# Optimization experiments

Measured on AMD Instinct MI355X. Metric: run time of the kernel, lower is better.

The kernel has to match this reference:

```python
import jax, jax.numpy as jnp
import numpy as np

B, T, C = 4, 2048, 1024
NH = 16
HD = C // NH  # 64


def setup_inputs() -> dict:
    key = jax.random.key(0)
    k1, k2, k3, k4, k5 = jax.random.split(key, 5)
    s_in = 1.0 / np.sqrt(C)
    return {
        "x": jax.random.normal(k1, (B, T, C), dtype=jnp.float32),
        "attention_mask": jnp.ones((B, T), dtype=jnp.float32),
        "W_qkv": jax.random.normal(k2, (C, 3 * C), dtype=jnp.float32) * s_in,
        "b_qkv": jnp.zeros((3 * C,), dtype=jnp.float32),
        "W_out": jax.random.normal(k3, (C, C), dtype=jnp.float32) * s_in,
        "b_out": jnp.zeros((C,), dtype=jnp.float32),
    }


def reference(x, attention_mask, W_qkv, b_qkv, W_out, b_out):
    Bx, Tx, Cx = x.shape
    # QKV projection: (B,T,3C)
    qkv = x @ W_qkv + b_qkv
    Q, K, V = jnp.split(qkv, 3, axis=-1)
    # (B, NH, T, HD)
    Q = Q.reshape(Bx, Tx, NH, HD).transpose(0, 2, 1, 3)
    K = K.reshape(Bx, Tx, NH, HD).transpose(0, 2, 1, 3)
    V = V.reshape(Bx, Tx, NH, HD).transpose(0, 2, 1, 3)
    # scaled scores (B, NH, T, T)
    scores = jnp.einsum("bhqd,bhkd->bhqk", Q, K) * (1.0 / np.sqrt(HD))
    # causal mask: set strictly-upper triangle to -inf (mask-fill semantics)
    causal = jnp.tril(jnp.ones((Tx, Tx), dtype=bool))[None, None]
    scores = jnp.where(causal, scores, -jnp.inf)
    # additive padding mask
    pad = (1.0 - attention_mask)[:, None, None, :] * jnp.finfo(scores.dtype).min
    scores = scores + pad
    attn = jax.nn.softmax(scores, axis=-1)
    # weighted values -> (B, T, C)
    wv = jnp.einsum("bhqk,bhkd->bhqd", attn, V)
    wv = wv.transpose(0, 2, 1, 3).reshape(Bx, Tx, Cx)
    return wv @ W_out + b_out
```

## Files before the change

kernel.cpp:

```cpp
#include <hip/hip_runtime.h>
#include <math.h>

constexpr int BB = 4;
constexpr int TT = 2048;
constexpr int CC = 1024;
constexpr int NHH = 16;
constexpr int HDD = 64;
constexpr int C3 = 3 * CC;

typedef __bf16 bf16x8 __attribute__((ext_vector_type(8)));
typedef float  f32x4  __attribute__((ext_vector_type(4)));

__device__ __forceinline__ unsigned short f2bf(float x) {
    union { float f; unsigned u; } v; v.f = x;
    unsigned r = v.u + 0x7fffu + ((v.u >> 16) & 1u);
    return (unsigned short)(r >> 16);
}

#define AS1(p) ((const __attribute__((address_space(1))) void*)(p))
#define AS3(p) ((__attribute__((address_space(3))) void*)(p))

__global__ __launch_bounds__(256) void cast_bf16(
    const float* __restrict__ src, unsigned short* __restrict__ dst, int n4)
{
    int i = blockIdx.x * 256 + threadIdx.x;
    if (i < n4) {
        float4 v = ((const float4*)src)[i];
        ushort4 o;
        o.x = f2bf(v.x); o.y = f2bf(v.y); o.z = f2bf(v.z); o.w = f2bf(v.w);
        ((ushort4*)dst)[i] = o;
    }
}

__global__ __launch_bounds__(256) void transpose_cast(
    const float* __restrict__ src, unsigned short* __restrict__ dst,
    int R, int Cn)
{
    __shared__ float tile[64][65];
    const int r0 = blockIdx.y * 64, c0 = blockIdx.x * 64;
    const int t = threadIdx.x;
    const int lr = t >> 4, lc = (t & 15) * 4;
    #pragma unroll
    for (int s = 0; s < 4; ++s) {
        float4 v = *(const float4*)&src[(size_t)(r0 + lr + s * 16) * Cn + c0 + lc];
        tile[lr + s * 16][lc + 0] = v.x;
        tile[lr + s * 16][lc + 1] = v.y;
        tile[lr + s * 16][lc + 2] = v.z;
        tile[lr + s * 16][lc + 3] = v.w;
    }
    __syncthreads();
    const int oi = t >> 2, oc = (t & 3) * 16;
    unsigned short buf[16];
    #pragma unroll
    for (int u = 0; u < 16; ++u)
        buf[u] = f2bf(tile[oc + u][oi]);
    unsigned short* d = &dst[(size_t)(c0 + oi) * R + r0 + oc];
    *(uint4*)(d + 0) = *(uint4*)&buf[0];
    *(uint4*)(d + 8) = *(uint4*)&buf[8];
}

template<bool BF16OUT, bool VSPLIT>
__global__ __launch_bounds__(256) void gemm_bt_mfma(
    const unsigned short* __restrict__ A,
    const unsigned short* __restrict__ Bt,
    const float* __restrict__ bias,
    void* __restrict__ OutV,
    unsigned short* __restrict__ Vt_g,
    int M, int N, int K, int scale_n, float scale)
{
    __shared__ alignas(16) unsigned short As[128 * 32];
    __shared__ alignas(16) unsigned short Bs[128 * 32];

    const int tid  = threadIdx.x;
    const int w    = tid >> 6;
    const int lane = tid & 63;
    const int quad = lane >> 4;
    const int col  = lane & 15;
    const int m0 = blockIdx.y * 128, n0 = blockIdx.x * 128;
    const int wr = w >> 1, wc = w & 1;

    f32x4 acc[4][4];
    #pragma unroll
    for (int i = 0; i < 4; ++i)
        #pragma unroll
        for (int j = 0; j < 4; ++j)
            #pragma unroll
            for (int r = 0; r < 4; ++r)
                acc[i][j][r] = 0.0f;

    const int sr = tid >> 2;
    const int sc = (tid & 3) * 8;
    char* AsB = (char*)As;
    char* BsB = (char*)Bs;

    const unsigned short* Ag0 = A  + (size_t)(m0 + sr) * K + sc;
    const unsigned short* Ag1 = A  + (size_t)(m0 + 64 + sr) * K + sc;
    const unsigned short* Bg0 = Bt + (size_t)(n0 + sr) * K + sc;
    const unsigned short* Bg1 = Bt + (size_t)(n0 + 64 + sr) * K + sc;

    for (int k0 = 0; k0 < K; k0 += 32) {
        if (k0) __syncthreads();
        __builtin_amdgcn_global_load_lds(AS1(Ag0 + k0), AS3(AsB + w * 1024),        16, 0, 0);
        __builtin_amdgcn_global_load_lds(AS1(Ag1 + k0), AS3(AsB + 4096 + w * 1024), 16, 0, 0);
        __builtin_amdgcn_global_load_lds(AS1(Bg0 + k0), AS3(BsB + w * 1024),        16, 0, 0);
        __builtin_amdgcn_global_load_lds(AS1(Bg1 + k0), AS3(BsB + 4096 + w * 1024), 16, 0, 0);
        __syncthreads();

        bf16x8 af[4], bf[4];
        #pragma unroll
        for (int i = 0; i < 4; ++i) {
            af[i] = *(const bf16x8*)&As[(wr * 64 + i * 16 + col) * 32 + quad * 8];
            bf[i] = *(const bf16x8*)&Bs[(wc * 64 + i * 16 + col) * 32 + quad * 8];
        }
        #pragma unroll
        for (int i = 0; i < 4; ++i)
            #pragma unroll
            for (int j = 0; j < 4; ++j)
                acc[i][j] = __builtin_amdgcn_mfma_f32_16x16x32_bf16(af[i], bf[j], acc[i][j], 0, 0, 0);
    }

    if (VSPLIT && n0 >= 2 * CC) {
        #pragma unroll
        for (int i = 0; i < 4; ++i) {
            const int mb   = m0 + wr * 64 + i * 16 + quad * 4;
            const int bidx = mb >> 11;
            const int tloc = mb & 2047;
            #pragma unroll
            for (int j = 0; j < 4; ++j) {
                const int n  = n0 + wc * 64 + j * 16 + col;
                const int hh = (n - 2 * CC) >> 6;
                const int dd = (n - 2 * CC) & 63;
                unsigned short pk[4];
                #pragma unroll
                for (int r = 0; r < 4; ++r)
                    pk[r] = f2bf(acc[i][j][r] + bias[n]);
                *(uint2*)&Vt_g[(((size_t)bidx * NHH + hh) * HDD + dd) * TT + tloc] =
                    *(const uint2*)pk;
            }
        }
    } else {
        #pragma unroll
        for (int i = 0; i < 4; ++i) {
            #pragma unroll
            for (int r = 0; r < 4; ++r) {
                const int m = m0 + wr * 64 + i * 16 + quad * 4 + r;
                #pragma unroll
                for (int j = 0; j < 4; ++j) {
                    const int n = n0 + wc * 64 + j * 16 + col;
                    float v = acc[i][j][r] + bias[n];
                    if (n < scale_n) v *= scale;
                    if (BF16OUT)
                        ((unsigned short*)OutV)[(size_t)m * N + n] = f2bf(v);
                    else
                        ((float*)OutV)[(size_t)m * N + n] = v;
                }
            }
        }
    }
}

constexpr int PP = 72;
constexpr float SM_MAX = 12.0f;

__global__ __launch_bounds__(512, 6) void attn_mfma(
    const unsigned short* __restrict__ QKV,
    const unsigned short* __restrict__ Vt_g,
    const float* __restrict__ amask,
    unsigned short* __restrict__ WV)
{
    __shared__ alignas(16) unsigned short Ks [2][64 * 64];
    __shared__ alignas(16) unsigned short Vts[2][64 * 64];
    __shared__ alignas(16) __bf16        Ps[8][16 * PP];

    const int tid  = threadIdx.x;
    const int w    = tid >> 6;
    const int lane = tid & 63;
    const int quad = lane >> 4;
    const int col  = lane & 15;
    const int bh = blockIdx.y, b = bh >> 4, h = bh & 15;
    const int jx = blockIdx.x;

    const size_t base = (size_t)b * TT * C3 + (size_t)h * HDD;
    const unsigned short* Qg = QKV + base;
    const unsigned short* Kg = QKV + base + CC;
    const unsigned short* Vt = Vt_g + (size_t)bh * HDD * TT;

    const int srow = tid >> 3;
    const int sch  = (tid & 7) ^ (srow & 7);
    const unsigned short* Ksrc = Kg + (size_t)srow * C3 + sch * 8;
    const unsigned short* Vsrc = Vt + (size_t)srow * TT + sch * 8;
    char* KsB  = (char*)&Ks[0][0];
    char* VtsB = (char*)&Vts[0][0];

    #pragma unroll
    for (int ph = 0; ph < 2; ++ph) {
        const int qb    = ph ? (15 - jx) : jx;
        const int qbase = qb * 128;
        const int qw    = qbase + w * 16;

        bf16x8 qf0 = *(const bf16x8*)(Qg + (size_t)(qw + col) * C3 + quad * 8);
        bf16x8 qf1 = *(const bf16x8*)(Qg + (size_t)(qw + col) * C3 + 32 + quad * 8);

        f32x4 o[4];
        float l[4];
        #pragma unroll
        for (int t = 0; t < 4; ++t)
            #pragma unroll
            for (int r = 0; r < 4; ++r) o[t][r] = 0.0f;
        #pragma unroll
        for (int r = 0; r < 4; ++r) l[r] = 0.0f;

        const int ntiles = (qbase >> 6) + 2;

        __builtin_amdgcn_global_load_lds(AS1(Ksrc), AS3(KsB  + w * 1024), 16, 0, 0);
        __builtin_amdgcn_global_load_lds(AS1(Vsrc), AS3(VtsB + w * 1024), 16, 0, 0);
        __syncthreads();

        for (int it = 0; it < ntiles; ++it) {
            const int kt  = it << 6;
            const int cur = it & 1;

            if (it + 1 < ntiles) {
                __builtin_amdgcn_global_load_lds(
                    AS1(Ksrc + (size_t)(kt + 64) * C3),
                    AS3(KsB + (cur ^ 1) * 8192 + w * 1024), 16, 0, 0);
                __builtin_amdgcn_global_load_lds(
                    AS1(Vsrc + (kt + 64)),
                    AS3(VtsB + (cur ^ 1) * 8192 + w * 1024), 16, 0, 0);
            }

            if (kt <= qw + 15) {
                const unsigned short* ksb = &Ks[cur][0];
                const unsigned short* vsb = &Vts[cur][0];

                f32x4 s[4];
                #pragma unroll
                for (int t = 0; t < 4; ++t) {
                    const int row = t * 16 + col;
                    const int c0 = (quad ^ (row & 7)) * 8;
                    const int c1 = ((quad + 4) ^ (row & 7)) * 8;
                    bf16x8 k0 = *(const bf16x8*)&ksb[row * 64 + c0];
                    bf16x8 k1 = *(const bf16x8*)&ksb[row * 64 + c1];
                    f32x4 z;
                    #pragma unroll
                    for (int r = 0; r < 4; ++r) z[r] = -SM_MAX;
                    z = __builtin_amdgcn_mfma_f32_16x16x32_bf16(qf0, k0, z, 0, 0, 0);
                    z = __builtin_amdgcn_mfma_f32_16x16x32_bf16(qf1, k1, z, 0, 0, 0);
                    s[t] = z;
                }

                const bool needc = (kt + 64 > qw);
                float mval[4];
                #pragma unroll
                for (int t = 0; t < 4; ++t)
                    mval[t] = amask[b * TT + kt + t * 16 + col];
                #pragma unroll
                for (int t = 0; t < 4; ++t) {
                    const int key = kt + t * 16 + col;
                    #pragma unroll
                    for (int r = 0; r < 4; ++r) {
                        float p = __expf(s[t][r]) * mval[t];
                        if (needc && key > qw + quad * 4 + r) p = 0.0f;
                        l[r] += p;
                        Ps[w][(quad * 4 + r) * PP + t * 16 + col] = (__bf16)p;
                    }
                }

                bf16x8 p0 = *(const bf16x8*)&Ps[w][col * PP + quad * 8];
                bf16x8 p1 = *(const bf16x8*)&Ps[w][col * PP + 32 + quad * 8];
                #pragma unroll
                for (int t = 0; t < 4; ++t) {
                    const int row = t * 16 + col;
                    const int c0 = (quad ^ (row & 7)) * 8;
                    const int c1 = ((quad + 4) ^ (row & 7)) * 8;
                    bf16x8 v0 = *(const bf16x8*)&vsb[row * 64 + c0];
                    bf16x8 v1 = *(const bf16x8*)&vsb[row * 64 + c1];
                    o[t] = __builtin_amdgcn_mfma_f32_16x16x32_bf16(p0, v0, o[t], 0, 0, 0);
                    o[t] = __builtin_amdgcn_mfma_f32_16x16x32_bf16(p1, v1, o[t], 0, 0, 0);
                }
            }
            __syncthreads();
        }

        #pragma unroll
        for (int off = 1; off < 16; off <<= 1)
            #pragma unroll
            for (int r = 0; r < 4; ++r)
                l[r] += __shfl_xor(l[r], off);
        #pragma unroll
        for (int r = 0; r < 4; ++r) {
            const float inv = 1.0f / l[r];
            const int q = qw + quad * 4 + r;
            unsigned short* dst = WV + ((size_t)b * TT + q) * CC + (size_t)h * HDD;
            #pragma unroll
            for (int t = 0; t < 4; ++t)
                dst[t * 16 + col] = f2bf(o[t][r] * inv);
        }
    }
}

extern "C" void kernel_launch(void* const* d_in, const int* in_sizes, int n_in,
                              void* d_out, int out_size, void* d_ws, size_t ws_size,
                              hipStream_t stream) {
    const float* x     = (const float*)d_in[0];
    const float* amask = (const float*)d_in[1];
    const float* Wqkv  = (const float*)d_in[2];
    const float* bqkv  = (const float*)d_in[3];
    const float* Wout  = (const float*)d_in[4];
    const float* bout  = (const float*)d_in[5];
    float* out = (float*)d_out;

    const int M = BB * TT;

    unsigned short* xb    = (unsigned short*)d_ws;
    unsigned short* Wqkvt = xb    + (size_t)M * CC;
    unsigned short* Woutt = Wqkvt + (size_t)C3 * CC;
    unsigned short* qkv   = Woutt + (size_t)CC * CC;
    unsigned short* wvb   = qkv   + (size_t)M * C3;
    unsigned short* Vt_g  = wvb   + (size_t)M * CC;

    dim3 blk(256);

    cast_bf16<<<dim3((M * CC / 4 + 255) / 256), blk, 0, stream>>>(x, xb, M * CC / 4);
    transpose_cast<<<dim3(C3 / 64, CC / 64), blk, 0, stream>>>(Wqkv, Wqkvt, CC, C3);
    transpose_cast<<<dim3(CC / 64, CC / 64), blk, 0, stream>>>(Wout, Woutt, CC, CC);

    gemm_bt_mfma<true, true><<<dim3(C3 / 128, M / 128), blk, 0, stream>>>(
        xb, Wqkvt, bqkv, qkv, Vt_g, M, C3, CC, CC, 0.125f);
    attn_mfma<<<dim3(TT / 256, BB * NHH), dim3(512), 0, stream>>>(qkv, Vt_g, amask, wvb);
    gemm_bt_mfma<false, false><<<dim3(CC / 128, M / 128), blk, 0, stream>>>(
        wvb, Woutt, bout, out, nullptr, M, CC, CC, 0, 1.0f);
}
```

Baseline: 284.2 us.

## Fuse prep kernels, double GEMM K-tile with swizzled LDS, fold log2e into Q scale

Merges the x cast and both weight transpose-casts into one prep launch, cutting launch overhead. The GEMM K-step grows from 32 to 64 with an XOR-swizzled LDS layout, halving barriers per K and avoiding bank conflicts, at the cost of twice the LDS per block. Attention now folds log2(e) into the Q scale and uses exp2f instead of __expf, with the fixed softmax offset rescaled to match. The larger LDS footprint may lower GEMM occupancy.

New measurement: 272.8 us. 4.0% less time.

```diff
diff --git a/kernel.cpp b/kernel.cpp
--- a/kernel.cpp
+++ b/kernel.cpp
@@ -20,25 +20,42 @@
 #define AS1(p) ((const __attribute__((address_space(1))) void*)(p))
 #define AS3(p) ((__attribute__((address_space(3))) void*)(p))
 
-__global__ __launch_bounds__(256) void cast_bf16(
-    const float* __restrict__ src, unsigned short* __restrict__ dst, int n4)
+constexpr int CAST_BLOCKS = (BB * TT * CC / 4) / 256;
+constexpr int TQKV_BLOCKS = (C3 / 64) * (CC / 64);
+constexpr int TOUT_BLOCKS = (CC / 64) * (CC / 64);
+
+__global__ __launch_bounds__(256) void prep(
+    const float* __restrict__ x,
+    const float* __restrict__ Wqkv,
+    const float* __restrict__ Wout,
+    unsigned short* __restrict__ xb,
+    unsigned short* __restrict__ Wqkvt,
+    unsigned short* __restrict__ Woutt)
 {
-    int i = blockIdx.x * 256 + threadIdx.x;
-    if (i < n4) {
-        float4 v = ((const float4*)src)[i];
+    __shared__ float tile[64][65];
+    const int bid = blockIdx.x;
+    const int t = threadIdx.x;
+
+    if (bid < CAST_BLOCKS) {
+        const int i = bid * 256 + t;
+        float4 v = ((const float4*)x)[i];
         ushort4 o;
         o.x = f2bf(v.x); o.y = f2bf(v.y); o.z = f2bf(v.z); o.w = f2bf(v.w);
-        ((ushort4*)dst)[i] = o;
-    }
-}
-
-__global__ __launch_bounds__(256) void transpose_cast(
-    const float* __restrict__ src, unsigned short* __restrict__ dst,
-    int R, int Cn)
-{
-    __shared__ float tile[64][65];
-    const int r0 = blockIdx.y * 64, c0 = blockIdx.x * 64;
-    const int t = threadIdx.x;
+        ((ushort4*)xb)[i] = o;
+        return;
+    }
+
+    const float* src; unsigned short* dst; int R, Cn, r0, c0;
+    if (bid < CAST_BLOCKS + TQKV_BLOCKS) {
+        const int tb = bid - CAST_BLOCKS;
+        src = Wqkv; dst = Wqkvt; R = CC; Cn = C3;
+        c0 = (tb % (C3 / 64)) * 64; r0 = (tb / (C3 / 64)) * 64;
+    } else {
+        const int tb = bid - CAST_BLOCKS - TQKV_BLOCKS;
+        src = Wout; dst = Woutt; R = CC; Cn = CC;
+        c0 = (tb % (CC / 64)) * 64; r0 = (tb / (CC / 64)) * 64;
+    }
+
     const int lr = t >> 4, lc = (t & 15) * 4;
     #pragma unroll
     for (int s = 0; s < 4; ++s) {
@@ -68,8 +85,8 @@
     unsigned short* __restrict__ Vt_g,
     int M, int N, int K, int scale_n, float scale)
 {
-    __shared__ alignas(16) unsigned short As[128 * 32];
-    __shared__ alignas(16) unsigned short Bs[128 * 32];
+    __shared__ alignas(16) unsigned short As[128 * 64];
+    __shared__ alignas(16) unsigned short Bs[128 * 64];
 
     const int tid  = threadIdx.x;
     const int w    = tid >> 6;
@@ -88,35 +105,44 @@
             for (int r = 0; r < 4; ++r)
                 acc[i][j][r] = 0.0f;
 
-    const int sr = tid >> 2;
-    const int sc = (tid & 3) * 8;
+    const int srow = tid >> 3;
+    const int spos = tid & 7;
     char* AsB = (char*)As;
     char* BsB = (char*)Bs;
 
-    const unsigned short* Ag0 = A  + (size_t)(m0 + sr) * K + sc;
-    const unsigned short* Ag1 = A  + (size_t)(m0 + 64 + sr) * K + sc;
-    const unsigned short* Bg0 = Bt + (size_t)(n0 + sr) * K + sc;
-    const unsigned short* Bg1 = Bt + (size_t)(n0 + 64 + sr) * K + sc;
-
-    for (int k0 = 0; k0 < K; k0 += 32) {
+    for (int k0 = 0; k0 < K; k0 += 64) {
         if (k0) __syncthreads();
-        __builtin_amdgcn_global_load_lds(AS1(Ag0 + k0), AS3(AsB + w * 1024),        16, 0, 0);
-        __builtin_amdgcn_global_load_lds(AS1(Ag1 + k0), AS3(AsB + 4096 + w * 1024), 16, 0, 0);
-        __builtin_amdgcn_global_load_lds(AS1(Bg0 + k0), AS3(BsB + w * 1024),        16, 0, 0);
-        __builtin_amdgcn_global_load_lds(AS1(Bg1 + k0), AS3(BsB + 4096 + w * 1024), 16, 0, 0);
+        #pragma unroll
+        for (int i = 0; i < 4; ++i) {
+            const int row = srow + 32 * i;
+            const int sch = spos ^ (row & 7);
+            __builtin_amdgcn_global_load_lds(
+                AS1(A + (size_t)(m0 + row) * K + k0 + sch * 8),
+                AS3(AsB + i * 4096 + w * 1024), 16, 0, 0);
+            __builtin_amdgcn_global_load_lds(
+                AS1(Bt + (size_t)(n0 + row) * K + k0 + sch * 8),
+                AS3(BsB + i * 4096 + w * 1024), 16, 0, 0);
+        }
         __syncthreads();
 
-        bf16x8 af[4], bf[4];
-        #pragma unroll
-        for (int i = 0; i < 4; ++i) {
-            af[i] = *(const bf16x8*)&As[(wr * 64 + i * 16 + col) * 32 + quad * 8];
-            bf[i] = *(const bf16x8*)&Bs[(wc * 64 + i * 16 + col) * 32 + quad * 8];
-        }
-        #pragma unroll
-        for (int i = 0; i < 4; ++i)
-            #pragma unroll
-            for (int j = 0; j < 4; ++j)
-                acc[i][j] = __builtin_amdgcn_mfma_f32_16x16x32_bf16(af[i], bf[j], acc[i][j], 0, 0, 0);
+        #pragma unroll
+        for (int ks = 0; ks < 2; ++ks) {
+            bf16x8 af[4], bf[4];
+            #pragma unroll
+            for (int i = 0; i < 4; ++i) {
+                const int ra = wr * 64 + i * 16 + col;
+                const int pa = ((quad + ks * 4) ^ (ra & 7)) * 8;
+                af[i] = *(const bf16x8*)&As[ra * 64 + pa];
+                const int rb = wc * 64 + i * 16 + col;
+                const int pb = ((quad + ks * 4) ^ (rb & 7)) * 8;
+                bf[i] = *(const bf16x8*)&Bs[rb * 64 + pb];
+            }
+            #pragma unroll
+            for (int i = 0; i < 4; ++i)
+                #pragma unroll
+                for (int j = 0; j < 4; ++j)
+                    acc[i][j] = __builtin_amdgcn_mfma_f32_16x16x32_bf16(af[i], bf[j], acc[i][j], 0, 0, 0);
+        }
     }
 
     if (VSPLIT && n0 >= 2 * CC) {
@@ -160,7 +186,7 @@
 }
 
 constexpr int PP = 72;
-constexpr float SM_MAX = 12.0f;
+constexpr float SM2 = 17.312340490667561f;
 
 __global__ __launch_bounds__(512, 6) void attn_mfma(
     const unsigned short* __restrict__ QKV,
@@ -243,7 +269,7 @@
                     bf16x8 k1 = *(const bf16x8*)&ksb[row * 64 + c1];
                     f32x4 z;
                     #pragma unroll
-                    for (int r = 0; r < 4; ++r) z[r] = -SM_MAX;
+                    for (int r = 0; r < 4; ++r) z[r] = -SM2;
                     z = __builtin_amdgcn_mfma_f32_16x16x32_bf16(qf0, k0, z, 0, 0, 0);
                     z = __builtin_amdgcn_mfma_f32_16x16x32_bf16(qf1, k1, z, 0, 0, 0);
                     s[t] = z;
@@ -259,7 +285,7 @@
                     const int key = kt + t * 16 + col;
                     #pragma unroll
                     for (int r = 0; r < 4; ++r) {
-                        float p = __expf(s[t][r]) * mval[t];
+                        float p = exp2f(s[t][r]) * mval[t];
                         if (needc && key > qw + quad * 4 + r) p = 0.0f;
                         l[r] += p;
                         Ps[w][(quad * 4 + r) * PP + t * 16 + col] = (__bf16)p;
@@ -321,12 +347,11 @@
 
     dim3 blk(256);
 
-    cast_bf16<<<dim3((M * CC / 4 + 255) / 256), blk, 0, stream>>>(x, xb, M * CC / 4);
-    transpose_cast<<<dim3(C3 / 64, CC / 64), blk, 0, stream>>>(Wqkv, Wqkvt, CC, C3);
-    transpose_cast<<<dim3(CC / 64, CC / 64), blk, 0, stream>>>(Wout, Woutt, CC, CC);
+    prep<<<dim3(CAST_BLOCKS + TQKV_BLOCKS + TOUT_BLOCKS), blk, 0, stream>>>(
+        x, Wqkv, Wout, xb, Wqkvt, Woutt);
 
     gemm_bt_mfma<true, true><<<dim3(C3 / 128, M / 128), blk, 0, stream>>>(
-        xb, Wqkvt, bqkv, qkv, Vt_g, M, C3, CC, CC, 0.125f);
+        xb, Wqkvt, bqkv, qkv, Vt_g, M, C3, CC, CC, 0.18033688011112043f);
     attn_mfma<<<dim3(TT / 256, BB * NHH), dim3(512), 0, stream>>>(qkv, Vt_g, amask, wvb);
     gemm_bt_mfma<false, false><<<dim3(CC / 128, M / 128), blk, 0, stream>>>(
         wvb, Woutt, bout, out, nullptr, M, CC, CC, 0, 1.0f);
```
